# Kernel tuning notes

Measured on AMD Instinct MI355X. Metric: run time of the kernel, lower is better.

The kernel has to match this reference:

```python
import jax, jax.numpy as jnp
import numpy as np

ALPHA = 0.2  # LeakyReLU negative slope

def setup_inputs() -> dict:
    key = jax.random.key(0)
    k1, k2 = jax.random.split(key)
    K, N = 4096, 1024
    x = jax.random.normal(k1, (K, N), dtype=jnp.float32)
    # xavier_uniform with gain 1.414 on shape (2N, 1)
    limit = 1.414 * np.sqrt(6.0 / (2 * N + 1))
    w = jax.random.uniform(k2, (2 * N, 1), dtype=jnp.float32, minval=-limit, maxval=limit)
    return {"x": x, "w": w}

def reference(x, w):
    # Faithful to: e[i,j] = leakyrelu(concat(x[i], x[j]) @ w)
    # Split w into halves -> outer-sum score (same math, no KxK x 2N intermediate).
    N = x.shape[1]
    w1 = w[:N, 0]   # (N,)
    w2 = w[N:, 0]   # (N,)
    s1 = x @ w1     # (K,)
    s2 = x @ w2     # (K,)
    e = jax.nn.leaky_relu(s1[:, None] + s2[None, :], negative_slope=ALPHA)  # (K, K)
    attention = jax.nn.softmax(e, axis=1)  # dropout p=0.0 -> identity
    h = attention @ x  # (K, N)
    return h
```

## Files before the change

kernel.cpp:

```cpp
#include <hip/hip_runtime.h>

#define KDIM 4096
#define NDIM 1024
#define ALPHA 0.2f
#define LOG2E 1.4426950408889634f
#define CCH 256
#define RCH 16
#define PFL 256

__device__ __align__(16) float g_s1L[KDIM];
__device__ __align__(16) float g_s2L[KDIM];
__device__ __align__(16) float g_E [2 * KDIM];
__device__ __align__(16) float g_F [2 * KDIM];
__device__ __align__(16) int   g_t  [KDIM];
__device__ __align__(16) int   g_sig[KDIM];
__device__ __align__(16) float g_cs [CCH][2 * NDIM];
__device__ __align__(16) float g_pre[CCH][2 * NDIM];
__device__ __align__(16) float g_tot[2 * NDIM];
__device__ __align__(16) float g_cz [2 * CCH];
__device__ __align__(16) float g_zpre[2 * CCH];
__device__ __align__(16) float g_ztot[2];
__device__ __align__(16) int g_sync[256 * 4 + 4];

__device__ __forceinline__ void ast8(float* p, float a, float b){
  float2 v = make_float2(a, b);
  unsigned long long u; __builtin_memcpy(&u, &v, 8);
  __hip_atomic_store((unsigned long long*)p, u, __ATOMIC_RELAXED,
                     __HIP_MEMORY_SCOPE_AGENT);
}
__device__ __forceinline__ float2 ald8(const float* p){
  unsigned long long u = __hip_atomic_load((const unsigned long long*)p,
                                           __ATOMIC_RELAXED, __HIP_MEMORY_SCOPE_AGENT);
  float2 v; __builtin_memcpy(&v, &u, 8); return v;
}
__device__ __forceinline__ void ast4f(float* p, float v){
  int u; __builtin_memcpy(&u, &v, 4);
  __hip_atomic_store((int*)p, u, __ATOMIC_RELAXED, __HIP_MEMORY_SCOPE_AGENT);
}
__device__ __forceinline__ float ald4f(const float* p){
  int u = __hip_atomic_load((const int*)p, __ATOMIC_RELAXED, __HIP_MEMORY_SCOPE_AGENT);
  float v; __builtin_memcpy(&v, &u, 4); return v;
}
__device__ __forceinline__ void ast4i(int* p, int v){
  __hip_atomic_store(p, v, __ATOMIC_RELAXED, __HIP_MEMORY_SCOPE_AGENT);
}
__device__ __forceinline__ int ald4i(const int* p){
  return __hip_atomic_load(p, __ATOMIC_RELAXED, __HIP_MEMORY_SCOPE_AGENT);
}

__device__ __forceinline__ void gbarrier(int epoch){
  __syncthreads();
  const int tid = threadIdx.x, bid = blockIdx.x;
  if (tid == 0){
    asm volatile("s_waitcnt vmcnt(0) lgkmcnt(0)" ::: "memory");
    __hip_atomic_store(&g_sync[bid * 4], epoch, __ATOMIC_RELAXED,
                       __HIP_MEMORY_SCOPE_AGENT);
  }
  if (bid == 0){
    while (__hip_atomic_load(&g_sync[tid * 4], __ATOMIC_RELAXED,
                             __HIP_MEMORY_SCOPE_AGENT) < epoch)
      __builtin_amdgcn_s_sleep(4);
    __syncthreads();
    if (tid == 0)
      __hip_atomic_store(&g_sync[1024], epoch, __ATOMIC_RELAXED,
                         __HIP_MEMORY_SCOPE_AGENT);
  } else if (tid == 0){
    while (__hip_atomic_load(&g_sync[1024], __ATOMIC_RELAXED,
                             __HIP_MEMORY_SCOPE_AGENT) < epoch)
      __builtin_amdgcn_s_sleep(8);
  }
  __syncthreads();
}

__global__ __launch_bounds__(256) void k_all(const float* __restrict__ x,
                                             const float* __restrict__ w,
                                             float* __restrict__ out){
  __shared__ __align__(16) union {
    float s2s[KDIM];
    struct { float TL[CCH][32]; float SS[8][32]; } d;
    struct {
      int    cnt[RCH + 1], off[RCH + 2], pos[RCH + 1];
      int    ilist[KDIM];
      float2 pfl[PFL];
    } e;
  } sh;
  __shared__ int   js [RCH];
  __shared__ float e1s[RCH], e2s[RCH];
  const int tid = threadIdx.x, lane = tid & 63, wv = tid >> 6;
  const int bid = blockIdx.x;

  {
    float4 W1r[4], W2r[4];
    #pragma unroll
    for (int q = 0; q < 4; ++q){
      const int o = q * 256 + lane * 4;
      W1r[q] = *(const float4*)(w + o);
      W2r[q] = *(const float4*)(w + NDIM + o);
    }
    const int wgid = bid * 4 + wv;
    #pragma unroll
    for (int rr = 0; rr < 4; ++rr){
      const int row = wgid * 4 + rr;
      const float* xr = x + (size_t)row * NDIM;
      float d1 = 0.f, d2 = 0.f;
      #pragma unroll
      for (int q = 0; q < 4; ++q){
        const float4 X = *(const float4*)(xr + q * 256 + lane * 4);
        d1 = fmaf(X.x, W1r[q].x, fmaf(X.y, W1r[q].y, fmaf(X.z, W1r[q].z, fmaf(X.w, W1r[q].w, d1))));
        d2 = fmaf(X.x, W2r[q].x, fmaf(X.y, W2r[q].y, fmaf(X.z, W2r[q].z, fmaf(X.w, W2r[q].w, d2))));
      }
      #pragma unroll
      for (int m = 32; m >= 1; m >>= 1){
        d1 += __shfl_xor(d1, m, 64);
        d2 += __shfl_xor(d2, m, 64);
      }
      if (lane == 0){
        const float s1 = d1 * LOG2E, s2 = d2 * LOG2E;
        ast4f(&g_s1L[row], s1);
        ast4f(&g_s2L[row], s2);
        ast8(&g_E[2 * row], __builtin_amdgcn_exp2f(s2),
                            __builtin_amdgcn_exp2f(ALPHA * s2));
        ast8(&g_F[2 * row], __builtin_amdgcn_exp2f(s1),
                            __builtin_amdgcn_exp2f(ALPHA * s1));
      }
    }
  }
  gbarrier(1);

  {
    #pragma unroll
    for (int q = 0; q < 8; ++q){
      const float2 v2 = ald8(&g_s2L[(q * 256 + tid) * 2]);
      ((float2*)sh.s2s)[q * 256 + tid] = v2;
    }
    __syncthreads();
    const int grp = tid >> 4, sub = tid & 15;
    #pragma unroll
    for (int pass = 0; pass < 2; ++pass){
      const int o = bid * 32 + pass * 16 + grp;
      int cnt = 0;
      if (o < KDIM){
        const float val = sh.s2s[o];
        #pragma unroll 4
        for (int m = 0; m < 64; ++m){
          const int q4 = m * 16 + sub;
          const float4 v4 = ((const float4*)sh.s2s)[q4];
          const int j0 = q4 * 4;
          cnt += (v4.x > val || (v4.x == val && (j0    ) < o));
          cnt += (v4.y > val || (v4.y == val && (j0 + 1) < o));
          cnt += (v4.z > val || (v4.z == val && (j0 + 2) < o));
          cnt += (v4.w > val || (v4.w == val && (j0 + 3) < o));
        }
      } else {
        const float thr = -ald4f(&g_s1L[o - KDIM]);
        #pragma unroll 4
        for (int m = 0; m < 64; ++m){
          const int q4 = m * 16 + sub;
          const float4 v4 = ((const float4*)sh.s2s)[q4];
          cnt += (v4.x >= thr) + (v4.y >= thr) + (v4.z >= thr) + (v4.w >= thr);
        }
      }
      cnt += __shfl_xor(cnt, 1, 64); cnt += __shfl_xor(cnt, 2, 64);
      cnt += __shfl_xor(cnt, 4, 64); cnt += __shfl_xor(cnt, 8, 64);
      if (sub == 0){
        if (o < KDIM) ast4i(&g_sig[cnt], o);
        else          ast4i(&g_t[o - KDIM], cnt);
      }
    }
  }
  gbarrier(2);

  {
    const int c = bid;
    if (tid < RCH){
      const int j = ald4i(&g_sig[c * RCH + tid]);
      js[tid]  = j;
      const float2 e = ald8(&g_E[2 * j]);
      e1s[tid] = e.x;
      e2s[tid] = e.y;
    }
    __syncthreads();
    if (tid == 0){
      float a = 0.f, b = 0.f;
      #pragma unroll
      for (int r = 0; r < RCH; ++r){ a += e1s[r]; b += e2s[r]; }
      ast8(&g_cz[2 * c], a, b);
    }
    float4 a1 = {0.f,0.f,0.f,0.f}, a2 = {0.f,0.f,0.f,0.f};
    #pragma unroll
    for (int r = 0; r < RCH; ++r){
      const float4 xv = *(const float4*)(x + (size_t)js[r] * NDIM + tid * 4);
      const float e1 = e1s[r], e2 = e2s[r];
      a1.x = fmaf(e1, xv.x, a1.x); a1.y = fmaf(e1, xv.y, a1.y);
      a1.z = fmaf(e1, xv.z, a1.z); a1.w = fmaf(e1, xv.w, a1.w);
      a2.x = fmaf(e2, xv.x, a2.x); a2.y = fmaf(e2, xv.y, a2.y);
      a2.z = fmaf(e2, xv.z, a2.z); a2.w = fmaf(e2, xv.w, a2.w);
    }
    ast8(&g_cs[c][tid * 4],            a1.x, a1.y);
    ast8(&g_cs[c][tid * 4 + 2],        a1.z, a1.w);
    ast8(&g_cs[c][NDIM + tid * 4],     a2.x, a2.y);
    ast8(&g_cs[c][NDIM + tid * 4 + 2], a2.z, a2.w);
  }
  gbarrier(3);

  if (bid < 64){
    const int s = tid >> 5, k2 = tid & 31;
    const int col = bid * 32 + k2;
    float run = 0.f;
    #pragma unroll 8
    for (int m = 0; m < 32; ++m){
      const float vv = ald4f(&g_cs[s * 32 + m][col]);
      sh.d.TL[s * 32 + m][k2] = vv;
      run += vv;
    }
    sh.d.SS[s][k2] = run;
    __syncthreads();
    if (s == 0){
      float acc = 0.f;
      #pragma unroll
      for (int t = 0; t < 8; ++t){
        const float vv = sh.d.SS[t][k2];
        sh.d.SS[t][k2] = acc;
        acc += vv;
      }
      ast4f(&g_tot[col], acc);
    }
    __syncthreads();
    run = sh.d.SS[s][k2];
    #pragma unroll 8
    for (int m = 0; m < 32; ++m){
      ast4f(&g_pre[s * 32 + m][col], run);
      run += sh.d.TL[s * 32 + m][k2];
    }
  } else if (bid == 64 && tid < 64){
    float v1[4], v2[4];
    #pragma unroll
    for (int q = 0; q < 4; ++q){
      const float2 e = ald8(&g_cz[2 * (tid * 4 + q)]);
      v1[q] = e.x; v2[q] = e.y;
    }
    const float s1 = v1[0] + v1[1] + v1[2] + v1[3];
    const float s2 = v2[0] + v2[1] + v2[2] + v2[3];
    float i1 = s1, i2 = s2;
    #pragma unroll
    for (int d = 1; d < 64; d <<= 1){
      const float t1 = __shfl_up(i1, d, 64);
      const float t2 = __shfl_up(i2, d, 64);
      if (tid >= d){ i1 += t1; i2 += t2; }
    }
    float e1 = i1 - s1, e2 = i2 - s2;
    #pragma unroll
    for (int q = 0; q < 4; ++q){
      ast8(&g_zpre[2 * (tid * 4 + q)], e1, e2);
      e1 += v1[q]; e2 += v2[q];
    }
    if (tid == 63) ast8(&g_ztot[0], e1, e2);
  }
  gbarrier(4);

  {
    const int c = bid;
    const bool last = (c == CCH - 1);
    const int nbuck = last ? RCH + 1 : RCH;
    if (tid <= RCH) sh.e.cnt[tid] = 0;
    __syncthreads();
    const int tbase = c * RCH;
    int myr[16];
    #pragma unroll
    for (int q = 0; q < 16; ++q){
      const int i = q * 256 + tid;
      const int t = ald4i(&g_t[i]);
      const int r = t - tbase;
      const bool in = (r >= 0) && (r < nbuck);
      myr[q] = in ? r : -1;
      if (in) atomicAdd(&sh.e.cnt[r], 1);
    }
    __syncthreads();
    if (tid == 0){
      int run = 0;
      #pragma unroll
      for (int r = 0; r <= RCH; ++r){
        const int vv = sh.e.cnt[r];
        sh.e.off[r] = run; sh.e.pos[r] = run;
        run += vv;
      }
      sh.e.off[RCH + 1] = run;
    }
    __syncthreads();
    #pragma unroll
    for (int q = 0; q < 16; ++q){
      if (myr[q] >= 0){
        const int i = q * 256 + tid;
        const int p = atomicAdd(&sh.e.pos[myr[q]], 1);
        sh.e.ilist[p] = i;
        if (p < PFL){
          const float2 pf = ald8(&g_F[2 * i]);
          sh.e.pfl[p] = pf;
        }
      }
    }
    __syncthreads();

    const float2 p1a = ald8(&g_pre[c][tid * 4]);
    const float2 p1b = ald8(&g_pre[c][tid * 4 + 2]);
    const float2 p2a = ald8(&g_pre[c][NDIM + tid * 4]);
    const float2 p2b = ald8(&g_pre[c][NDIM + tid * 4 + 2]);
    float4 a1 = make_float4(p1a.x, p1a.y, p1b.x, p1b.y);
    float4 a2 = make_float4(p2a.x, p2a.y, p2b.x, p2b.y);
    const float2 t2a = ald8(&g_tot[NDIM + tid * 4]);
    const float2 t2b = ald8(&g_tot[NDIM + tid * 4 + 2]);
    const float4 t2 = make_float4(t2a.x, t2a.y, t2b.x, t2b.y);
    const float2 zp = ald8(&g_zpre[2 * c]);
    float za1 = zp.x, za2 = zp.y;
    const float zt2 = ald8(&g_ztot[0]).y;
    float4 v[RCH];
    #pragma unroll
    for (int r = 0; r < RCH; ++r)
      v[r] = *(const float4*)(x + (size_t)js[r] * NDIM + tid * 4);

    #pragma unroll
    for (int r = 0; r < RCH; ++r){
      for (int e = sh.e.off[r]; e < sh.e.off[r + 1]; ++e){
        const int i = sh.e.ilist[e];
        float F1, F2;
        if (e < PFL){ const float2 pf = sh.e.pfl[e]; F1 = pf.x; F2 = pf.y; }
        else        { const float2 pf = ald8(&g_F[2 * i]); F1 = pf.x; F2 = pf.y; }
        const float rz = 1.0f / fmaf(F1, za1, F2 * (zt2 - za2));
        float4 h;
        h.x = fmaf(F1, a1.x, F2 * (t2.x - a2.x)) * rz;
        h.y = fmaf(F1, a1.y, F2 * (t2.y - a2.y)) * rz;
        h.z = fmaf(F1, a1.z, F2 * (t2.z - a2.z)) * rz;
        h.w = fmaf(F1, a1.w, F2 * (t2.w - a2.w)) * rz;
        *(float4*)(out + (size_t)i * NDIM + tid * 4) = h;
      }
      const float e1 = e1s[r], e2 = e2s[r];
      za1 += e1; za2 += e2;
      const float4 xv = v[r];
      a1.x = fmaf(e1, xv.x, a1.x); a1.y = fmaf(e1, xv.y, a1.y);
      a1.z = fmaf(e1, xv.z, a1.z); a1.w = fmaf(e1, xv.w, a1.w);
      a2.x = fmaf(e2, xv.x, a2.x); a2.y = fmaf(e2, xv.y, a2.y);
      a2.z = fmaf(e2, xv.z, a2.z); a2.w = fmaf(e2, xv.w, a2.w);
    }
    if (last){
      for (int e = sh.e.off[RCH]; e < sh.e.off[RCH + 1]; ++e){
        const int i = sh.e.ilist[e];
        float F1, F2;
        if (e < PFL){ const float2 pf = sh.e.pfl[e]; F1 = pf.x; F2 = pf.y; }
        else        { const float2 pf = ald8(&g_F[2 * i]); F1 = pf.x; F2 = pf.y; }
        const float rz = 1.0f / fmaf(F1, za1, F2 * (zt2 - za2));
        float4 h;
        h.x = fmaf(F1, a1.x, F2 * (t2.x - a2.x)) * rz;
        h.y = fmaf(F1, a1.y, F2 * (t2.y - a2.y)) * rz;
        h.z = fmaf(F1, a1.z, F2 * (t2.z - a2.z)) * rz;
        h.w = fmaf(F1, a1.w, F2 * (t2.w - a2.w)) * rz;
        *(float4*)(out + (size_t)i * NDIM + tid * 4) = h;
      }
    }
  }
}

extern "C" void kernel_launch(void* const* d_in, const int* in_sizes, int n_in,
                              void* d_out, int out_size, void* d_ws, size_t ws_size,
                              hipStream_t stream){
  const float* x = (const float*)d_in[0];
  const float* w = (const float*)d_in[1];
  float* out = (float*)d_out;
  (void)in_sizes; (void)n_in; (void)out_size; (void)d_ws; (void)ws_size;

  static void* sync_addr = nullptr;
  if (!sync_addr) (void)hipGetSymbolAddress(&sync_addr, HIP_SYMBOL(g_sync));
  (void)hipMemsetAsync(sync_addr, 0, (256 * 4 + 4) * sizeof(int), stream);
  k_all<<<dim3(256), dim3(256), 0, stream>>>(x, w, out);
}
```

Baseline: 119.3 us.

## Quadruple persistent grid to 1024 blocks and split column work per chunk

Result: faster. 116.9 us (-2.1%).

```diff
diff --git a/kernel.cpp b/kernel.cpp
--- a/kernel.cpp
+++ b/kernel.cpp
@@ -7,6 +7,7 @@
 #define CCH 256
 #define RCH 16
 #define PFL 256
+#define GRID 1024
 
 __device__ __align__(16) float g_s1L[KDIM];
 __device__ __align__(16) float g_s2L[KDIM];
@@ -18,9 +19,7 @@
 __device__ __align__(16) float g_pre[CCH][2 * NDIM];
 __device__ __align__(16) float g_tot[2 * NDIM];
 __device__ __align__(16) float g_cz [2 * CCH];
-__device__ __align__(16) float g_zpre[2 * CCH];
-__device__ __align__(16) float g_ztot[2];
-__device__ __align__(16) int g_sync[256 * 4 + 4];
+__device__ __align__(16) int g_sync[GRID * 4 + 4];
 
 __device__ __forceinline__ void ast8(float* p, float a, float b){
   float2 v = make_float2(a, b);
@@ -57,15 +56,18 @@
                        __HIP_MEMORY_SCOPE_AGENT);
   }
   if (bid == 0){
-    while (__hip_atomic_load(&g_sync[tid * 4], __ATOMIC_RELAXED,
-                             __HIP_MEMORY_SCOPE_AGENT) < epoch)
-      __builtin_amdgcn_s_sleep(4);
+    #pragma unroll
+    for (int s = 0; s < 4; ++s){
+      while (__hip_atomic_load(&g_sync[(s * 256 + tid) * 4], __ATOMIC_RELAXED,
+                               __HIP_MEMORY_SCOPE_AGENT) < epoch)
+        __builtin_amdgcn_s_sleep(4);
+    }
     __syncthreads();
     if (tid == 0)
-      __hip_atomic_store(&g_sync[1024], epoch, __ATOMIC_RELAXED,
+      __hip_atomic_store(&g_sync[GRID * 4], epoch, __ATOMIC_RELAXED,
                          __HIP_MEMORY_SCOPE_AGENT);
   } else if (tid == 0){
-    while (__hip_atomic_load(&g_sync[1024], __ATOMIC_RELAXED,
+    while (__hip_atomic_load(&g_sync[GRID * 4], __ATOMIC_RELAXED,
                              __HIP_MEMORY_SCOPE_AGENT) < epoch)
       __builtin_amdgcn_s_sleep(8);
   }
@@ -84,8 +86,9 @@
       float2 pfl[PFL];
     } e;
   } sh;
-  __shared__ int   js [RCH];
-  __shared__ float e1s[RCH], e2s[RCH];
+  __shared__ int    js [RCH];
+  __shared__ float  e1s[RCH], e2s[RCH];
+  __shared__ float4 zred[4];
   const int tid = threadIdx.x, lane = tid & 63, wv = tid >> 6;
   const int bid = blockIdx.x;
 
@@ -97,32 +100,28 @@
       W1r[q] = *(const float4*)(w + o);
       W2r[q] = *(const float4*)(w + NDIM + o);
     }
-    const int wgid = bid * 4 + wv;
-    #pragma unroll
-    for (int rr = 0; rr < 4; ++rr){
-      const int row = wgid * 4 + rr;
-      const float* xr = x + (size_t)row * NDIM;
-      float d1 = 0.f, d2 = 0.f;
-      #pragma unroll
-      for (int q = 0; q < 4; ++q){
-        const float4 X = *(const float4*)(xr + q * 256 + lane * 4);
-        d1 = fmaf(X.x, W1r[q].x, fmaf(X.y, W1r[q].y, fmaf(X.z, W1r[q].z, fmaf(X.w, W1r[q].w, d1))));
-        d2 = fmaf(X.x, W2r[q].x, fmaf(X.y, W2r[q].y, fmaf(X.z, W2r[q].z, fmaf(X.w, W2r[q].w, d2))));
-      }
-      #pragma unroll
-      for (int m = 32; m >= 1; m >>= 1){
-        d1 += __shfl_xor(d1, m, 64);
-        d2 += __shfl_xor(d2, m, 64);
-      }
-      if (lane == 0){
-        const float s1 = d1 * LOG2E, s2 = d2 * LOG2E;
-        ast4f(&g_s1L[row], s1);
-        ast4f(&g_s2L[row], s2);
-        ast8(&g_E[2 * row], __builtin_amdgcn_exp2f(s2),
-                            __builtin_amdgcn_exp2f(ALPHA * s2));
-        ast8(&g_F[2 * row], __builtin_amdgcn_exp2f(s1),
-                            __builtin_amdgcn_exp2f(ALPHA * s1));
-      }
+    const int row = bid * 4 + wv;
+    const float* xr = x + (size_t)row * NDIM;
+    float d1 = 0.f, d2 = 0.f;
+    #pragma unroll
+    for (int q = 0; q < 4; ++q){
+      const float4 X = *(const float4*)(xr + q * 256 + lane * 4);
+      d1 = fmaf(X.x, W1r[q].x, fmaf(X.y, W1r[q].y, fmaf(X.z, W1r[q].z, fmaf(X.w, W1r[q].w, d1))));
+      d2 = fmaf(X.x, W2r[q].x, fmaf(X.y, W2r[q].y, fmaf(X.z, W2r[q].z, fmaf(X.w, W2r[q].w, d2))));
+    }
+    #pragma unroll
+    for (int m = 32; m >= 1; m >>= 1){
+      d1 += __shfl_xor(d1, m, 64);
+      d2 += __shfl_xor(d2, m, 64);
+    }
+    if (lane == 0){
+      const float s1 = d1 * LOG2E, s2 = d2 * LOG2E;
+      ast4f(&g_s1L[row], s1);
+      ast4f(&g_s2L[row], s2);
+      ast8(&g_E[2 * row], __builtin_amdgcn_exp2f(s2),
+                          __builtin_amdgcn_exp2f(ALPHA * s2));
+      ast8(&g_F[2 * row], __builtin_amdgcn_exp2f(s1),
+                          __builtin_amdgcn_exp2f(ALPHA * s1));
     }
   }
   gbarrier(1);
@@ -134,44 +133,42 @@
       ((float2*)sh.s2s)[q * 256 + tid] = v2;
     }
     __syncthreads();
-    const int grp = tid >> 4, sub = tid & 15;
-    #pragma unroll
-    for (int pass = 0; pass < 2; ++pass){
-      const int o = bid * 32 + pass * 16 + grp;
-      int cnt = 0;
-      if (o < KDIM){
-        const float val = sh.s2s[o];
-        #pragma unroll 4
-        for (int m = 0; m < 64; ++m){
-          const int q4 = m * 16 + sub;
-          const float4 v4 = ((const float4*)sh.s2s)[q4];
-          const int j0 = q4 * 4;
-          cnt += (v4.x > val || (v4.x == val && (j0    ) < o));
-          cnt += (v4.y > val || (v4.y == val && (j0 + 1) < o));
-          cnt += (v4.z > val || (v4.z == val && (j0 + 2) < o));
-          cnt += (v4.w > val || (v4.w == val && (j0 + 3) < o));
-        }
-      } else {
-        const float thr = -ald4f(&g_s1L[o - KDIM]);
-        #pragma unroll 4
-        for (int m = 0; m < 64; ++m){
-          const int q4 = m * 16 + sub;
-          const float4 v4 = ((const float4*)sh.s2s)[q4];
-          cnt += (v4.x >= thr) + (v4.y >= thr) + (v4.z >= thr) + (v4.w >= thr);
-        }
-      }
-      cnt += __shfl_xor(cnt, 1, 64); cnt += __shfl_xor(cnt, 2, 64);
-      cnt += __shfl_xor(cnt, 4, 64); cnt += __shfl_xor(cnt, 8, 64);
-      if (sub == 0){
-        if (o < KDIM) ast4i(&g_sig[cnt], o);
-        else          ast4i(&g_t[o - KDIM], cnt);
-      }
+    const int grp = tid >> 5, sub = tid & 31;
+    const int o = bid * 8 + grp;
+    int cnt = 0;
+    if (o < KDIM){
+      const float val = sh.s2s[o];
+      #pragma unroll 4
+      for (int m = 0; m < 32; ++m){
+        const int q4 = m * 32 + sub;
+        const float4 v4 = ((const float4*)sh.s2s)[q4];
+        const int j0 = q4 * 4;
+        cnt += (v4.x > val || (v4.x == val && (j0    ) < o));
+        cnt += (v4.y > val || (v4.y == val && (j0 + 1) < o));
+        cnt += (v4.z > val || (v4.z == val && (j0 + 2) < o));
+        cnt += (v4.w > val || (v4.w == val && (j0 + 3) < o));
+      }
+    } else {
+      const float thr = -ald4f(&g_s1L[o - KDIM]);
+      #pragma unroll 4
+      for (int m = 0; m < 32; ++m){
+        const int q4 = m * 32 + sub;
+        const float4 v4 = ((const float4*)sh.s2s)[q4];
+        cnt += (v4.x >= thr) + (v4.y >= thr) + (v4.z >= thr) + (v4.w >= thr);
+      }
+    }
+    cnt += __shfl_xor(cnt, 1, 64);  cnt += __shfl_xor(cnt, 2, 64);
+    cnt += __shfl_xor(cnt, 4, 64);  cnt += __shfl_xor(cnt, 8, 64);
+    cnt += __shfl_xor(cnt, 16, 64);
+    if (sub == 0){
+      if (o < KDIM) ast4i(&g_sig[cnt], o);
+      else          ast4i(&g_t[o - KDIM], cnt);
     }
   }
   gbarrier(2);
 
   {
-    const int c = bid;
+    const int c = bid >> 2, qt = bid & 3;
     if (tid < RCH){
       const int j = ald4i(&g_sig[c * RCH + tid]);
       js[tid]  = j;
@@ -180,26 +177,22 @@
       e2s[tid] = e.y;
     }
     __syncthreads();
-    if (tid == 0){
+    if (qt == 0 && tid == 0){
       float a = 0.f, b = 0.f;
       #pragma unroll
       for (int r = 0; r < RCH; ++r){ a += e1s[r]; b += e2s[r]; }
       ast8(&g_cz[2 * c], a, b);
     }
-    float4 a1 = {0.f,0.f,0.f,0.f}, a2 = {0.f,0.f,0.f,0.f};
+    const int col = qt * 256 + tid;
+    float a1 = 0.f, a2 = 0.f;
     #pragma unroll
     for (int r = 0; r < RCH; ++r){
-      const float4 xv = *(const float4*)(x + (size_t)js[r] * NDIM + tid * 4);
-      const float e1 = e1s[r], e2 = e2s[r];
-      a1.x = fmaf(e1, xv.x, a1.x); a1.y = fmaf(e1, xv.y, a1.y);
-      a1.z = fmaf(e1, xv.z, a1.z); a1.w = fmaf(e1, xv.w, a1.w);
-      a2.x = fmaf(e2, xv.x, a2.x); a2.y = fmaf(e2, xv.y, a2.y);
-      a2.z = fmaf(e2, xv.z, a2.z); a2.w = fmaf(e2, xv.w, a2.w);
-    }
-    ast8(&g_cs[c][tid * 4],            a1.x, a1.y);
-    ast8(&g_cs[c][tid * 4 + 2],        a1.z, a1.w);
-    ast8(&g_cs[c][NDIM + tid * 4],     a2.x, a2.y);
-    ast8(&g_cs[c][NDIM + tid * 4 + 2], a2.z, a2.w);
+      const float xv = x[(size_t)js[r] * NDIM + col];
+      a1 = fmaf(e1s[r], xv, a1);
+      a2 = fmaf(e2s[r], xv, a2);
+    }
+    ast4f(&g_cs[c][col], a1);
+    ast4f(&g_cs[c][NDIM + col], a2);
   }
   gbarrier(3);
 
@@ -232,38 +225,33 @@
       ast4f(&g_pre[s * 32 + m][col], run);
       run += sh.d.TL[s * 32 + m][k2];
     }
-  } else if (bid == 64 && tid < 64){
-    float v1[4], v2[4];
-    #pragma unroll
-    for (int q = 0; q < 4; ++q){
-      const float2 e = ald8(&g_cz[2 * (tid * 4 + q)]);
-      v1[q] = e.x; v2[q] = e.y;
-    }
-    const float s1 = v1[0] + v1[1] + v1[2] + v1[3];
-    const float s2 = v2[0] + v2[1] + v2[2] + v2[3];
-    float i1 = s1, i2 = s2;
-    #pragma unroll
-    for (int d = 1; d < 64; d <<= 1){
-      const float t1 = __shfl_up(i1, d, 64);
-      const float t2 = __shfl_up(i2, d, 64);
-      if (tid >= d){ i1 += t1; i2 += t2; }
-    }
-    float e1 = i1 - s1, e2 = i2 - s2;
-    #pragma unroll
-    for (int q = 0; q < 4; ++q){
-      ast8(&g_zpre[2 * (tid * 4 + q)], e1, e2);
-      e1 += v1[q]; e2 += v2[q];
-    }
-    if (tid == 63) ast8(&g_ztot[0], e1, e2);
   }
   gbarrier(4);
 
   {
-    const int c = bid;
+    const int c = bid >> 2, qt = bid & 3;
     const bool last = (c == CCH - 1);
     const int nbuck = last ? RCH + 1 : RCH;
+
+    const float2 ez = ald8(&g_cz[2 * tid]);
+    float zp1 = (tid < c) ? ez.x : 0.f;
+    float zp2 = (tid < c) ? ez.y : 0.f;
+    float zt2p = ez.y;
+    #pragma unroll
+    for (int m = 32; m >= 1; m >>= 1){
+      zp1  += __shfl_xor(zp1,  m, 64);
+      zp2  += __shfl_xor(zp2,  m, 64);
+      zt2p += __shfl_xor(zt2p, m, 64);
+    }
+    if (lane == 0) zred[wv] = make_float4(zp1, zp2, zt2p, 0.f);
     if (tid <= RCH) sh.e.cnt[tid] = 0;
     __syncthreads();
+    float za1 = 0.f, za2 = 0.f, zt2 = 0.f;
+    #pragma unroll
+    for (int w2 = 0; w2 < 4; ++w2){
+      za1 += zred[w2].x; za2 += zred[w2].y; zt2 += zred[w2].z;
+    }
+
     const int tbase = c * RCH;
     int myr[16];
     #pragma unroll
@@ -301,22 +289,14 @@
     }
     __syncthreads();
 
-    const float2 p1a = ald8(&g_pre[c][tid * 4]);
-    const float2 p1b = ald8(&g_pre[c][tid * 4 + 2]);
-    const float2 p2a = ald8(&g_pre[c][NDIM + tid * 4]);
-    const float2 p2b = ald8(&g_pre[c][NDIM + tid * 4 + 2]);
-    float4 a1 = make_float4(p1a.x, p1a.y, p1b.x, p1b.y);
-    float4 a2 = make_float4(p2a.x, p2a.y, p2b.x, p2b.y);
-    const float2 t2a = ald8(&g_tot[NDIM + tid * 4]);
-    const float2 t2b = ald8(&g_tot[NDIM + tid * 4 + 2]);
-    const float4 t2 = make_float4(t2a.x, t2a.y, t2b.x, t2b.y);
-    const float2 zp = ald8(&g_zpre[2 * c]);
-    float za1 = zp.x, za2 = zp.y;
-    const float zt2 = ald8(&g_ztot[0]).y;
-    float4 v[RCH];
+    const int col = qt * 256 + tid;
+    float a1 = ald4f(&g_pre[c][col]);
+    float a2 = ald4f(&g_pre[c][NDIM + col]);
+    const float t2 = ald4f(&g_tot[NDIM + col]);
+    float v[RCH];
     #pragma unroll
     for (int r = 0; r < RCH; ++r)
-      v[r] = *(const float4*)(x + (size_t)js[r] * NDIM + tid * 4);
+      v[r] = x[(size_t)js[r] * NDIM + col];
 
     #pragma unroll
     for (int r = 0; r < RCH; ++r){
@@ -326,20 +306,11 @@
         if (e < PFL){ const float2 pf = sh.e.pfl[e]; F1 = pf.x; F2 = pf.y; }
         else        { const float2 pf = ald8(&g_F[2 * i]); F1 = pf.x; F2 = pf.y; }
         const float rz = 1.0f / fmaf(F1, za1, F2 * (zt2 - za2));
-        float4 h;
-        h.x = fmaf(F1, a1.x, F2 * (t2.x - a2.x)) * rz;
-        h.y = fmaf(F1, a1.y, F2 * (t2.y - a2.y)) * rz;
-        h.z = fmaf(F1, a1.z, F2 * (t2.z - a2.z)) * rz;
-        h.w = fmaf(F1, a1.w, F2 * (t2.w - a2.w)) * rz;
-        *(float4*)(out + (size_t)i * NDIM + tid * 4) = h;
-      }
-      const float e1 = e1s[r], e2 = e2s[r];
-      za1 += e1; za2 += e2;
-      const float4 xv = v[r];
-      a1.x = fmaf(e1, xv.x, a1.x); a1.y = fmaf(e1, xv.y, a1.y);
-      a1.z = fmaf(e1, xv.z, a1.z); a1.w = fmaf(e1, xv.w, a1.w);
-      a2.x = fmaf(e2, xv.x, a2.x); a2.y = fmaf(e2, xv.y, a2.y);
-      a2.z = fmaf(e2, xv.z, a2.z); a2.w = fmaf(e2, xv.w, a2.w);
+        out[(size_t)i * NDIM + col] = fmaf(F1, a1, F2 * (t2 - a2)) * rz;
+      }
+      za1 += e1s[r]; za2 += e2s[r];
+      a1 = fmaf(e1s[r], v[r], a1);
+      a2 = fmaf(e2s[r], v[r], a2);
     }
     if (last){
       for (int e = sh.e.off[RCH]; e < sh.e.off[RCH + 1]; ++e){
@@ -348,12 +319,7 @@
         if (e < PFL){ const float2 pf = sh.e.pfl[e]; F1 = pf.x; F2 = pf.y; }
         else        { const float2 pf = ald8(&g_F[2 * i]); F1 = pf.x; F2 = pf.y; }
         const float rz = 1.0f / fmaf(F1, za1, F2 * (zt2 - za2));
-        float4 h;
-        h.x = fmaf(F1, a1.x, F2 * (t2.x - a2.x)) * rz;
-        h.y = fmaf(F1, a1.y, F2 * (t2.y - a2.y)) * rz;
-        h.z = fmaf(F1, a1.z, F2 * (t2.z - a2.z)) * rz;
-        h.w = fmaf(F1, a1.w, F2 * (t2.w - a2.w)) * rz;
-        *(float4*)(out + (size_t)i * NDIM + tid * 4) = h;
+        out[(size_t)i * NDIM + col] = fmaf(F1, a1, F2 * (t2 - a2)) * rz;
       }
     }
   }
@@ -369,6 +335,6 @@
 
   static void* sync_addr = nullptr;
   if (!sync_addr) (void)hipGetSymbolAddress(&sync_addr, HIP_SYMBOL(g_sync));
-  (void)hipMemsetAsync(sync_addr, 0, (256 * 4 + 4) * sizeof(int), stream);
-  k_all<<<dim3(256), dim3(256), 0, stream>>>(x, w, out);
-}
+  (void)hipMemsetAsync(sync_addr, 0, (GRID * 4 + 4) * sizeof(int), stream);
+  k_all<<<dim3(GRID), dim3(256), 0, stream>>>(x, w, out);
+}
```
